# Kernel tuning notes

Measured on AMD Instinct MI355X. Metric: run time of the kernel, lower is better.

Reference implementation:

```python
import jax, jax.numpy as jnp
import numpy as np

L, C, F, K = 8192, 2048, 128, 257  # timesteps, input_size, filter_size, lag (odd => symmetric 'same' pad)
NY = 256  # number of overwritten channel rows


def setup_inputs() -> dict:
    key = jax.random.key(0)
    k1, k2, k3, k4 = jax.random.split(key, 4)
    x = jax.random.normal(k1, (L, C), dtype=jnp.float32)
    Yt = jax.random.randint(k2, (NY,), 0, C)
    # learned parameters (torch.rand -> uniform[0,1))
    g = jax.random.uniform(k3, (C, F), dtype=jnp.float32)
    kernel = jax.random.uniform(k4, (F, K), dtype=jnp.float32)
    return {"x": x, "Yt": Yt, "g": g, "kernel": kernel}


def reference(x, Yt, g, kernel):
    # synapse[c] is the per-channel 1D filter; the original builds a dense
    # (C, C, K) kernel whose only non-zero slices are the diagonal, so the
    # full conv1d is mathematically a depthwise (grouped) conv.
    synapse = jnp.matmul(g, kernel)          # (C, K)
    lhs = x.T[None]                          # (1, C, L)  NCH
    rhs = synapse[:, None, :]                # (C, 1, K)  OIH, groups=C
    pad = (kernel.shape[1] - 1) // 2         # torch padding='same', odd K
    out = jax.lax.conv_general_dilated(
        lhs, rhs,
        window_strides=(1,),
        padding=[(pad, pad)],
        feature_group_count=x.shape[1],
        dimension_numbers=("NCH", "OIH", "NCH"),
    )                                        # (1, C, L)
    # result[:, Yt, :] = x.T[Yt] : scatter-overwrite selected channel rows
    out = out.at[:, Yt, :].set(x.T[Yt][None])
    return out
```

## Files before the change

### kernel.cpp

```cpp
#include <hip/hip_runtime.h>

#define LL   8192
#define CC   2048
#define FF   128
#define KK   257
#define PAD  128

#define SROWP 328
#define NT   18

#define ROWS 1280

typedef __bf16 bf16x8 __attribute__((ext_vector_type(8)));
typedef float  f32x16 __attribute__((ext_vector_type(16)));

static __device__ __forceinline__ unsigned short f2bf(float f) {
    unsigned u = __float_as_uint(f);
    u = (u + 0x7fffu + ((u >> 16) & 1u)) >> 16;
    return (unsigned short)u;
}

__global__ __launch_bounds__(256) void synb_kernel(const float* __restrict__ g,
                                                   const float* __restrict__ kern,
                                                   const int* __restrict__ Yt, int ny,
                                                   unsigned short* __restrict__ synEb) {
    __shared__ int sfl[4];
    const int c0 = blockIdx.x * 4;
    const int t  = threadIdx.x;
    if (t < 4) sfl[t] = 0;
    __syncthreads();
    for (int i = t; i < ny; i += 256) {
        int y = Yt[i];
        #pragma unroll
        for (int ii = 0; ii < 4; ++ii) if (y == c0 + ii) sfl[ii] = 1;
    }
    __syncthreads();
    const float* g0 = g + (size_t)(c0 + 0) * FF;
    const float* g1 = g + (size_t)(c0 + 1) * FF;
    const float* g2 = g + (size_t)(c0 + 2) * FF;
    const float* g3 = g + (size_t)(c0 + 3) * FF;
    const int fl0 = sfl[0], fl1 = sfl[1], fl2 = sfl[2], fl3 = sfl[3];
    for (int p = t; p < SROWP; p += 256) {
        const int kk = p - 32;
        float a0 = 0.f, a1 = 0.f, a2 = 0.f, a3 = 0.f;
        const bool inr = (kk >= 0) && (kk < KK);
        if (inr) {
            #pragma unroll 8
            for (int f = 0; f < FF; ++f) {
                float kv = kern[f * KK + kk];
                a0 += kv * g0[f];
                a1 += kv * g1[f];
                a2 += kv * g2[f];
                a3 += kv * g3[f];
            }
        }
        float dlt = (kk == PAD) ? 1.f : 0.f;
        float v0 = inr ? (fl0 ? dlt : a0) : 0.f;
        float v1 = inr ? (fl1 ? dlt : a1) : 0.f;
        float v2 = inr ? (fl2 ? dlt : a2) : 0.f;
        float v3 = inr ? (fl3 ? dlt : a3) : 0.f;
        synEb[(size_t)(c0 + 0) * SROWP + p] = f2bf(v0);
        synEb[(size_t)(c0 + 1) * SROWP + p] = f2bf(v1);
        synEb[(size_t)(c0 + 2) * SROWP + p] = f2bf(v2);
        synEb[(size_t)(c0 + 3) * SROWP + p] = f2bf(v3);
    }
}

__global__ __launch_bounds__(256, 4) void fused_conv(const float* __restrict__ x,
                                                     const unsigned short* __restrict__ synEb,
                                                     float* __restrict__ out) {
    __shared__ alignas(16) unsigned short xch[16][ROWS];
    const int t  = threadIdx.x;
    const int W0 = blockIdx.x << 10;
    const int c0 = blockIdx.y << 4;

    #pragma unroll
    for (int k = 0; k < 10; ++k) {
        int pidx = (k << 8) + t;
        int ch4  = pidx & 3;
        int pp   = pidx >> 2;
        int lg   = W0 + (pp << 1) - 128;
        const float* sp = x + (size_t)lg * CC + c0 + (ch4 << 2);
        float4 ve = make_float4(0.f, 0.f, 0.f, 0.f);
        float4 vo = make_float4(0.f, 0.f, 0.f, 0.f);
        if ((unsigned)lg       < (unsigned)LL) ve = *(const float4*)sp;
        if ((unsigned)(lg + 1) < (unsigned)LL) vo = *(const float4*)(sp + CC);
        int gq = pp >> 2;
        int gp = gq ^ ((gq >> 3) & 7);
        int dw = (gp << 2) | (pp & 3);
        const float* pe = (const float*)&ve;
        const float* po = (const float*)&vo;
        #pragma unroll
        for (int c2 = 0; c2 < 4; ++c2) {
            unsigned val = (unsigned)f2bf(pe[c2]) | ((unsigned)f2bf(po[c2]) << 16);
            ((unsigned*)xch[(ch4 << 2) + c2])[dw] = val;
        }
    }
    __syncthreads();

    const int w = t >> 6, ln = t & 63;
    const int j = ln & 31, q = ln >> 5;
    const int bb  = (q << 4) - 2 * j + 64;
    const int dwb = bb >> 2;
    const int sh  = (bb & 2) << 3;
    const int gb  = (j << 2) + q;

    for (int cc = 0; cc < 4; ++cc) {
        const int ci = (w << 2) + cc;
        const unsigned* rp = (const unsigned*)(synEb + (size_t)(c0 + ci) * SROWP) + dwb;
        f32x16 acc;
        #pragma unroll
        for (int r = 0; r < 16; ++r) acc[r] = 0.f;
        #pragma unroll
        for (int m = 0; m < NT; ++m) {
            unsigned w0 = rp[(m << 3) + 0], w1 = rp[(m << 3) + 1], w2 = rp[(m << 3) + 2],
                     w3 = rp[(m << 3) + 3], w4 = rp[(m << 3) + 4];
            union { unsigned d[4]; bf16x8 v; } B;
            B.d[0] = (unsigned)((((unsigned long long)w1 << 32) | w0) >> sh);
            B.d[1] = (unsigned)((((unsigned long long)w2 << 32) | w1) >> sh);
            B.d[2] = (unsigned)((((unsigned long long)w3 << 32) | w2) >> sh);
            B.d[3] = (unsigned)((((unsigned long long)w4 << 32) | w3) >> sh);
            int gq = gb + (m << 1);
            int gp = gq ^ ((gq >> 3) & 7);
            union { int4 i4; bf16x8 v; } A;
            A.i4 = *(const int4*)(&xch[ci][gp << 3]);
            acc = __builtin_amdgcn_mfma_f32_32x32x16_bf16(A.v, B.v, acc, 0, 0, 0);
        }
        float* o = out + (size_t)(c0 + ci) * LL + W0 + j;
        #pragma unroll
        for (int r = 0; r < 16; ++r) {
            int row = (r & 3) + ((r >> 2) << 3) + (q << 2);
            o[row << 5] = acc[r];
        }
    }
}

extern "C" void kernel_launch(void* const* d_in, const int* in_sizes, int n_in,
                              void* d_out, int out_size, void* d_ws, size_t ws_size,
                              hipStream_t stream) {
    const float* x    = (const float*)d_in[0];
    const int*   Yt   = (const int*)  d_in[1];
    const float* g    = (const float*)d_in[2];
    const float* kern = (const float*)d_in[3];
    float* out = (float*)d_out;
    const int ny = in_sizes[1];

    unsigned short* synEb = (unsigned short*)d_ws;

    synb_kernel<<<CC / 4, 256, 0, stream>>>(g, kern, Yt, ny, synEb);
    fused_conv<<<dim3(LL / 1024, CC / 16), 256, 0, stream>>>(x, synEb, out);
}
```

Before: 152.5 us.

## Pipeline x tiles with double-buffered LDS across persistent 4-window loop

```diff
diff --git a/kernel.cpp b/kernel.cpp
--- a/kernel.cpp
+++ b/kernel.cpp
@@ -8,8 +8,9 @@
 
 #define SROWP 328
 #define NT   18
-
-#define ROWS 1280
+#define NCH  8
+#define NW   4
+#define ROWS 1288
 
 typedef __bf16 bf16x8 __attribute__((ext_vector_type(8)));
 typedef float  f32x16 __attribute__((ext_vector_type(16)));
@@ -66,72 +67,115 @@
     }
 }
 
-__global__ __launch_bounds__(256, 4) void fused_conv(const float* __restrict__ x,
-                                                     const unsigned short* __restrict__ synEb,
-                                                     float* __restrict__ out) {
-    __shared__ alignas(16) unsigned short xch[16][ROWS];
-    const int t  = threadIdx.x;
-    const int W0 = blockIdx.x << 10;
-    const int c0 = blockIdx.y << 4;
-
+static __device__ __forceinline__ void stage_issue(const float* __restrict__ x,
+                                                   int W0, int c0, int t,
+                                                   float4* ev, float4* ov) {
     #pragma unroll
-    for (int k = 0; k < 10; ++k) {
+    for (int k = 0; k < 5; ++k) {
         int pidx = (k << 8) + t;
-        int ch4  = pidx & 3;
-        int pp   = pidx >> 2;
+        int ch4  = pidx & 1;
+        int pp   = pidx >> 1;
         int lg   = W0 + (pp << 1) - 128;
         const float* sp = x + (size_t)lg * CC + c0 + (ch4 << 2);
-        float4 ve = make_float4(0.f, 0.f, 0.f, 0.f);
-        float4 vo = make_float4(0.f, 0.f, 0.f, 0.f);
-        if ((unsigned)lg       < (unsigned)LL) ve = *(const float4*)sp;
-        if ((unsigned)(lg + 1) < (unsigned)LL) vo = *(const float4*)(sp + CC);
-        int gq = pp >> 2;
-        int gp = gq ^ ((gq >> 3) & 7);
-        int dw = (gp << 2) | (pp & 3);
-        const float* pe = (const float*)&ve;
-        const float* po = (const float*)&vo;
+        float4 a = make_float4(0.f, 0.f, 0.f, 0.f);
+        float4 b = make_float4(0.f, 0.f, 0.f, 0.f);
+        if ((unsigned)lg       < (unsigned)LL) a = *(const float4*)sp;
+        if ((unsigned)(lg + 1) < (unsigned)LL) b = *(const float4*)(sp + CC);
+        ev[k] = a; ov[k] = b;
+    }
+}
+
+static __device__ __forceinline__ void stage_write(unsigned short (*buf)[ROWS], int t,
+                                                   const float4* ev, const float4* ov) {
+    #pragma unroll
+    for (int k = 0; k < 5; ++k) {
+        int pidx = (k << 8) + t;
+        int ch4  = pidx & 1;
+        int pp   = pidx >> 1;
+        int gq   = pp >> 2;
+        int gp   = gq ^ ((gq >> 3) & 7);
+        int dw   = (gp << 2) | (pp & 3);
+        const float* pe = (const float*)&ev[k];
+        const float* po = (const float*)&ov[k];
         #pragma unroll
         for (int c2 = 0; c2 < 4; ++c2) {
             unsigned val = (unsigned)f2bf(pe[c2]) | ((unsigned)f2bf(po[c2]) << 16);
-            ((unsigned*)xch[(ch4 << 2) + c2])[dw] = val;
+            ((unsigned*)buf[(ch4 << 2) + c2])[dw] = val;
         }
     }
-    __syncthreads();
+}
 
-    const int w = t >> 6, ln = t & 63;
+__global__ __launch_bounds__(256, 2) void fused_conv(const float* __restrict__ x,
+                                                     const unsigned short* __restrict__ synEb,
+                                                     float* __restrict__ out) {
+    __shared__ alignas(16) unsigned short xch[2][NCH][ROWS];
+    __shared__ alignas(16) unsigned short synL[NCH][SROWP];
+    const int t = threadIdx.x;
+
+    const int d    = (blockIdx.y << 1) | blockIdx.x;
+    const int grp  = ((d >> 6) << 3) | (d & 7);
+    const int rnk  = (d >> 3) & 7;
+    const int cg   = (grp << 2) | (rnk >> 1);
+    const int bx   = rnk & 1;
+    const int c0 = cg << 3;
+    const int L0 = bx << 12;
+
+    {
+        const int rr = t >> 5, u0 = t & 31;
+        const unsigned* src = (const unsigned*)(synEb + (size_t)(c0 + rr) * SROWP);
+        unsigned* dst = (unsigned*)synL[rr];
+        for (int u = u0; u < SROWP / 2; u += 32) dst[u] = src[u];
+    }
+
+    const int w_id = t >> 6, ln = t & 63;
     const int j = ln & 31, q = ln >> 5;
     const int bb  = (q << 4) - 2 * j + 64;
     const int dwb = bb >> 2;
     const int sh  = (bb & 2) << 3;
     const int gb  = (j << 2) + q;
 
-    for (int cc = 0; cc < 4; ++cc) {
-        const int ci = (w << 2) + cc;
-        const unsigned* rp = (const unsigned*)(synEb + (size_t)(c0 + ci) * SROWP) + dwb;
-        f32x16 acc;
+    float4 ev[5], ov[5];
+    stage_issue(x, L0, c0, t, ev, ov);
+    stage_write(xch[0], t, ev, ov);
+    __syncthreads();
+
+    for (int w = 0; w < NW; ++w) {
+        const int cur = w & 1;
+        const int W0  = L0 + (w << 10);
+        if (w + 1 < NW) stage_issue(x, W0 + 1024, c0, t, ev, ov);
+
         #pragma unroll
-        for (int r = 0; r < 16; ++r) acc[r] = 0.f;
-        #pragma unroll
-        for (int m = 0; m < NT; ++m) {
-            unsigned w0 = rp[(m << 3) + 0], w1 = rp[(m << 3) + 1], w2 = rp[(m << 3) + 2],
-                     w3 = rp[(m << 3) + 3], w4 = rp[(m << 3) + 4];
-            union { unsigned d[4]; bf16x8 v; } B;
-            B.d[0] = (unsigned)((((unsigned long long)w1 << 32) | w0) >> sh);
-            B.d[1] = (unsigned)((((unsigned long long)w2 << 32) | w1) >> sh);
-            B.d[2] = (unsigned)((((unsigned long long)w3 << 32) | w2) >> sh);
-            B.d[3] = (unsigned)((((unsigned long long)w4 << 32) | w3) >> sh);
-            int gq = gb + (m << 1);
-            int gp = gq ^ ((gq >> 3) & 7);
-            union { int4 i4; bf16x8 v; } A;
-            A.i4 = *(const int4*)(&xch[ci][gp << 3]);
-            acc = __builtin_amdgcn_mfma_f32_32x32x16_bf16(A.v, B.v, acc, 0, 0, 0);
+        for (int cc = 0; cc < 2; ++cc) {
+            const int ci = (w_id << 1) + cc;
+            const unsigned* rp = (const unsigned*)(synL[ci]) + dwb;
+            f32x16 acc;
+            #pragma unroll
+            for (int r = 0; r < 16; ++r) acc[r] = 0.f;
+            #pragma unroll
+            for (int m = 0; m < NT; ++m) {
+                unsigned w0 = rp[(m << 3) + 0], w1 = rp[(m << 3) + 1], w2 = rp[(m << 3) + 2],
+                         w3 = rp[(m << 3) + 3], w4 = rp[(m << 3) + 4];
+                union { unsigned dd[4]; bf16x8 v; } B;
+                B.dd[0] = (unsigned)((((unsigned long long)w1 << 32) | w0) >> sh);
+                B.dd[1] = (unsigned)((((unsigned long long)w2 << 32) | w1) >> sh);
+                B.dd[2] = (unsigned)((((unsigned long long)w3 << 32) | w2) >> sh);
+                B.dd[3] = (unsigned)((((unsigned long long)w4 << 32) | w3) >> sh);
+                int gq2 = gb + (m << 1);
+                int gp2 = gq2 ^ ((gq2 >> 3) & 7);
+                union { int4 i4; bf16x8 v; } A;
+                A.i4 = *(const int4*)(&xch[cur][ci][gp2 << 3]);
+                acc = __builtin_amdgcn_mfma_f32_32x32x16_bf16(A.v, B.v, acc, 0, 0, 0);
+            }
+            float* o = out + (size_t)(c0 + ci) * LL + W0 + j;
+            #pragma unroll
+            for (int r = 0; r < 16; ++r) {
+                int row = (r & 3) + ((r >> 2) << 3) + (q << 2);
+                o[row << 5] = acc[r];
+            }
         }
-        float* o = out + (size_t)(c0 + ci) * LL + W0 + j;
-        #pragma unroll
-        for (int r = 0; r < 16; ++r) {
-            int row = (r & 3) + ((r >> 2) << 3) + (q << 2);
-            o[row << 5] = acc[r];
-        }
+        __syncthreads();
+        if (w + 1 < NW) stage_write(xch[cur ^ 1], t, ev, ov);
+        __syncthreads();
     }
 }
 
@@ -148,5 +192,5 @@
     unsigned short* synEb = (unsigned short*)d_ws;
 
     synb_kernel<<<CC / 4, 256, 0, stream>>>(g, kern, Yt, ny, synEb);
-    fused_conv<<<dim3(LL / 1024, CC / 16), 256, 0, stream>>>(x, synEb, out);
+    fused_conv<<<dim3(2, 256), 256, 0, stream>>>(x, synEb, out);
 }
```

New measurement: 157.4 us. 1.03x slower.
